# Optimization experiments

Measured on AMD Instinct MI355X. Metric: run time of the kernel, lower is better.

The kernel has to match this reference:

```python
import jax, jax.numpy as jnp
import numpy as np

N, E = 50000, 800000
D, H = 256, 256
OA, OS, OE = 21, 2, 5


def _sage(x, src, dst, wl, bl, wr):
    # PyG SAGEConv: out = lin_l(mean_{j in N(i)} x_j) + lin_r(x_i); bias lives in lin_l
    n = x.shape[0]
    msg = x[src]                                            # [E, d] gather
    agg = jax.ops.segment_sum(msg, dst, num_segments=n)     # [N, d]
    cnt = jax.ops.segment_sum(jnp.ones((src.shape[0],), x.dtype), dst, num_segments=n)
    mean = agg / jnp.maximum(cnt, 1.0)[:, None]
    return mean @ wl.T + bl + x @ wr.T


def _bn(x, g, b, eps=1e-5):
    mu = x.mean(axis=0)
    var = x.var(axis=0)
    return (x - mu) * jax.lax.rsqrt(var + eps) * g + b


def setup_inputs() -> dict:
    key = jax.random.key(0)
    ks = jax.random.split(key, 32)

    def lin(k, o, i):
        s = 1.0 / np.sqrt(i)
        k1, k2 = jax.random.split(k)
        return (jax.random.uniform(k1, (o, i), jnp.float32, -s, s),
                jax.random.uniform(k2, (o,), jnp.float32, -s, s))

    w1l, b1 = lin(ks[3], H, D); w1r, _ = lin(ks[4], H, D)
    w2l, b2 = lin(ks[5], H, H); w2r, _ = lin(ks[6], H, H)
    w3l, b3 = lin(ks[7], H, H); w3r, _ = lin(ks[8], H, H)
    wal, ba = lin(ks[9], OA, H); war, _ = lin(ks[10], OA, H)
    wsl, bs = lin(ks[11], OS, H); wsr, _ = lin(ks[12], OS, H)
    wel, be = lin(ks[13], OE, H); wer, _ = lin(ks[14], OE, H)

    return {
        'x': jax.random.normal(ks[0], (N, D), jnp.float32),
        'edge_src': jax.random.randint(ks[1], (E,), 0, N),
        'edge_dst': jax.random.randint(ks[2], (E,), 0, N),
        'w1l': w1l, 'b1': b1, 'w1r': w1r, 'g1': jnp.ones((H,), jnp.float32), 'bt1': jnp.zeros((H,), jnp.float32),
        'w2l': w2l, 'b2': b2, 'w2r': w2r, 'g2': jnp.ones((H,), jnp.float32), 'bt2': jnp.zeros((H,), jnp.float32),
        'w3l': w3l, 'b3': b3, 'w3r': w3r, 'g3': jnp.ones((H,), jnp.float32), 'bt3': jnp.zeros((H,), jnp.float32),
        'wal': wal, 'ba': ba, 'war': war,
        'wsl': wsl, 'bs': bs, 'wsr': wsr,
        'wel': wel, 'be': be, 'wer': wer,
    }


def reference(x, edge_src, edge_dst,
              w1l, b1, w1r, g1, bt1,
              w2l, b2, w2r, g2, bt2,
              w3l, b3, w3r, g3, bt3,
              wal, ba, war, wsl, bs, wsr, wel, be, wer):
    h = jax.nn.relu(_bn(_sage(x, edge_src, edge_dst, w1l, b1, w1r), g1, bt1))
    h = jax.nn.relu(_bn(_sage(h, edge_src, edge_dst, w2l, b2, w2r), g2, bt2))
    h = jax.nn.relu(_bn(_sage(h, edge_src, edge_dst, w3l, b3, w3r), g3, bt3))
    # dropout is identity in eval mode
    age = _sage(h, edge_src, edge_dst, wal, ba, war)
    sex = _sage(h, edge_src, edge_dst, wsl, bs, wsr)
    eth = _sage(h, edge_src, edge_dst, wel, be, wer)
    return age, sex, eth
```

## Files before the change

kernel.cpp:

```cpp
#include <hip/hip_runtime.h>
#include <hip/hip_bf16.h>
#include <cstddef>

#define HD 256
#define KD 512
#define NH 28

typedef __attribute__((ext_vector_type(8))) short bf16x8;
typedef __attribute__((ext_vector_type(4))) float f32x4;

__device__ inline float bf2f(unsigned short u) { return __uint_as_float(((unsigned)u) << 16); }
__device__ inline unsigned short f2bf(float f) {
    __hip_bfloat16 h = __float2bfloat16(f);
    return *(unsigned short*)&h;
}
__device__ inline float qmax_col(float g, float bt) { return fmaxf(bt + 5.2f * fabsf(g), 1e-6f); }
#define XLO  (-5.5f)
#define XRNG (11.0f)

__global__ void hist_kernel(const int* __restrict__ dst, int* __restrict__ cnt, int E) {
    int e = blockIdx.x * blockDim.x + threadIdx.x;
    if (e < E) atomicAdd(&cnt[dst[e]], 1);
}

__global__ void chunk_reduce_kernel(const int* __restrict__ cnt, int* __restrict__ bsum, int n) {
    __shared__ int sdata[4];
    int idx = blockIdx.x * 256 + threadIdx.x;
    int v = (idx < n) ? ((cnt[idx] + 7) & ~7) : 0;
    for (int off = 32; off > 0; off >>= 1) v += __shfl_down(v, off, 64);
    int lane = threadIdx.x & 63, wv = threadIdx.x >> 6;
    if (lane == 0) sdata[wv] = v;
    __syncthreads();
    if (threadIdx.x == 0) bsum[blockIdx.x] = sdata[0] + sdata[1] + sdata[2] + sdata[3];
}

__global__ void scan_chunks_kernel(const int* __restrict__ bsum, int* __restrict__ boff,
                                   int nchunks, int* __restrict__ row_ptr_end) {
    int t = threadIdx.x;
    int v = (t < nchunks) ? bsum[t] : 0;
    int lane = t & 63, wv = t >> 6;
    int incl = v;
    for (int off = 1; off < 64; off <<= 1) { int u = __shfl_up(incl, off, 64); if (lane >= off) incl += u; }
    __shared__ int wsum[4];
    if (lane == 63) wsum[wv] = incl;
    __syncthreads();
    int base = 0;
    for (int w2 = 0; w2 < 4; ++w2) if (w2 < wv) base += wsum[w2];
    if (t < nchunks) boff[t] = base + incl - v;
    if (t == nchunks - 1) *row_ptr_end = base + incl;
}

__global__ void scan_final_kernel(const int* __restrict__ cnt, const int* __restrict__ boff,
                                  int* __restrict__ row_ptr, float* __restrict__ invdeg, int n) {
    int idx = blockIdx.x * 256 + threadIdx.x;
    int v = (idx < n) ? cnt[idx] : 0;
    int pv = (v + 7) & ~7;
    int lane = threadIdx.x & 63, wv = threadIdx.x >> 6;
    int incl = pv;
    for (int off = 1; off < 64; off <<= 1) { int u = __shfl_up(incl, off, 64); if (lane >= off) incl += u; }
    __shared__ int wsum[4];
    if (lane == 63) wsum[wv] = incl;
    __syncthreads();
    int base = 0;
    for (int w2 = 0; w2 < 4; ++w2) if (w2 < wv) base += wsum[w2];
    if (idx < n) {
        row_ptr[idx] = boff[blockIdx.x] + base + incl - pv;
        invdeg[idx] = 1.0f / fmaxf((float)v, 1.0f);
    }
}

__global__ void scatter_kernel(const int* __restrict__ src, const int* __restrict__ dst,
                               const int* __restrict__ row_ptr, int* __restrict__ cursor,
                               int* __restrict__ col_idx, int E) {
    int e = blockIdx.x * blockDim.x + threadIdx.x;
    if (e < E) {
        int d = dst[e];
        int pos = atomicAdd(&cursor[d], 1);
        col_idx[row_ptr[d] + pos] = src[e];
    }
}

__global__ void fill_pad_kernel(const int* __restrict__ cnt, const int* __restrict__ row_ptr,
                                int* __restrict__ col_idx, int n) {
    int idx = blockIdx.x * 256 + threadIdx.x;
    if (idx >= n) return;
    int s = row_ptr[idx] + cnt[idx];
    int e = row_ptr[idx + 1];
    for (; s < e; ++s) col_idx[s] = n;
}

__global__ void pack_all(const float* __restrict__ w1l, const float* __restrict__ w1r,
                         const float* __restrict__ w2l, const float* __restrict__ w2r,
                         const float* __restrict__ w3l, const float* __restrict__ w3r,
                         const float* __restrict__ wal, const float* __restrict__ war,
                         const float* __restrict__ wsl, const float* __restrict__ wsr,
                         const float* __restrict__ wel, const float* __restrict__ wer,
                         const float* __restrict__ ba, const float* __restrict__ bs,
                         const float* __restrict__ be,
                         unsigned short* __restrict__ wc1, unsigned short* __restrict__ wc2,
                         unsigned short* __restrict__ wc3, unsigned short* __restrict__ w2h,
                         float* __restrict__ bcat) {
    int idx = blockIdx.x * 256 + threadIdx.x;
    if (idx < 3 * HD * KD) {
        int l = idx / (HD * KD), r = idx % (HD * KD);
        int nn = r >> 9, k = r & 511;
        const float* L = (l == 0) ? w1l : (l == 1) ? w2l : w3l;
        const float* R = (l == 0) ? w1r : (l == 1) ? w2r : w3r;
        float v = (k < HD) ? L[nn * HD + k] : R[nn * HD + (k - HD)];
        unsigned short* D = (l == 0) ? wc1 : (l == 1) ? wc2 : wc3;
        D[r] = f2bf(v);
        return;
    }
    int r = idx - 3 * HD * KD;
    if (r >= 64 * HD) return;
    int o = r >> 8, k = r & 255;
    float v = 0.f;
    if (o < 21)                    v = wal[o * HD + k];
    else if (o < 23)               v = wsl[(o - 21) * HD + k];
    else if (o < 28)               v = wel[(o - 23) * HD + k];
    else if (o >= 32 && o < 53)    v = war[(o - 32) * HD + k];
    else if (o >= 53 && o < 55)    v = wsr[(o - 53) * HD + k];
    else if (o >= 55 && o < 60)    v = wer[(o - 55) * HD + k];
    w2h[r] = f2bf(v);
    if (k == 0 && o < 32) {
        float b = 0.f;
        if (o < 21) b = ba[o]; else if (o < 23) b = bs[o - 21]; else if (o < 28) b = be[o - 23];
        bcat[o] = b;
    }
}

__global__ void convert_x_kernel(const float* __restrict__ x, unsigned short* __restrict__ buf,
                                 unsigned* __restrict__ q8, int n) {
    int idx = blockIdx.x * 256 + threadIdx.x;
    if (idx >= n * 64) return;
    int r = idx >> 6, c = idx & 63;
    float4 v = ((const float4*)x)[idx];
    ushort4 o;
    o.x = f2bf(v.x); o.y = f2bf(v.y); o.z = f2bf(v.z); o.w = f2bf(v.w);
    *(ushort4*)&buf[(size_t)r * KD + HD + c * 4] = o;
    const float si = 255.f / XRNG;
    unsigned q0 = (unsigned)fminf(fmaxf((v.x - XLO) * si + 0.5f, 0.f), 255.f);
    unsigned q1 = (unsigned)fminf(fmaxf((v.y - XLO) * si + 0.5f, 0.f), 255.f);
    unsigned q2 = (unsigned)fminf(fmaxf((v.z - XLO) * si + 0.5f, 0.f), 255.f);
    unsigned q3 = (unsigned)fminf(fmaxf((v.w - XLO) * si + 0.5f, 0.f), 255.f);
    q8[(size_t)r * 64 + c] = q0 | (q1 << 8) | (q2 << 16) | (q3 << 24);
}

__device__ inline void agg_u8_core(const unsigned* __restrict__ src,
                                   const int* __restrict__ col_idx, int s, int e,
                                   float& fa0, float& fa1, float& fa2, float& fa3) {
    fa0 = fa1 = fa2 = fa3 = 0.f;
    int i = s;
    while (i < e) {
        int ce = i + 256; if (ce > e) ce = e;
        unsigned acc02 = 0, acc13 = 0;
        for (; i < ce; i += 8) {
            int4 ja = *(const int4*)&col_idx[i];
            int4 jb = *(const int4*)&col_idx[i + 4];
            unsigned w0 = src[(size_t)ja.x << 6];
            unsigned w1 = src[(size_t)ja.y << 6];
            unsigned w2 = src[(size_t)ja.z << 6];
            unsigned w3 = src[(size_t)ja.w << 6];
            unsigned w4 = src[(size_t)jb.x << 6];
            unsigned w5 = src[(size_t)jb.y << 6];
            unsigned w6 = src[(size_t)jb.z << 6];
            unsigned w7 = src[(size_t)jb.w << 6];
            acc02 += w0 & 0x00ff00ffu; acc13 += (w0 >> 8) & 0x00ff00ffu;
            acc02 += w1 & 0x00ff00ffu; acc13 += (w1 >> 8) & 0x00ff00ffu;
            acc02 += w2 & 0x00ff00ffu; acc13 += (w2 >> 8) & 0x00ff00ffu;
            acc02 += w3 & 0x00ff00ffu; acc13 += (w3 >> 8) & 0x00ff00ffu;
            acc02 += w4 & 0x00ff00ffu; acc13 += (w4 >> 8) & 0x00ff00ffu;
            acc02 += w5 & 0x00ff00ffu; acc13 += (w5 >> 8) & 0x00ff00ffu;
            acc02 += w6 & 0x00ff00ffu; acc13 += (w6 >> 8) & 0x00ff00ffu;
            acc02 += w7 & 0x00ff00ffu; acc13 += (w7 >> 8) & 0x00ff00ffu;
        }
        fa0 += (float)(acc02 & 0xffffu); fa2 += (float)(acc02 >> 16);
        fa1 += (float)(acc13 & 0xffffu); fa3 += (float)(acc13 >> 16);
    }
}

__global__ __launch_bounds__(256) void agg_mean_u8x(unsigned short* __restrict__ buf,
                                                    const unsigned* __restrict__ q8,
                                                    const int* __restrict__ row_ptr,
                                                    const int* __restrict__ col_idx,
                                                    const float* __restrict__ invdeg, int n) {
    int wv = threadIdx.x >> 6, lane = threadIdx.x & 63;
    int node = blockIdx.x * 4 + wv;
    if (node >= n) return;
    int s = row_ptr[node], e = row_ptr[node + 1];
    float fa0, fa1, fa2, fa3;
    agg_u8_core(q8 + lane, col_idx, s, e, fa0, fa1, fa2, fa3);
    float inv = invdeg[node] * (XRNG / 255.f);
    float off = (s < e) ? XLO : 0.f;
    ushort4 o;
    o.x = f2bf(fa0 * inv + off);
    o.y = f2bf(fa1 * inv + off);
    o.z = f2bf(fa2 * inv + off);
    o.w = f2bf(fa3 * inv + off);
    *(ushort4*)&buf[(size_t)node * KD + lane * 4] = o;
}

__global__ __launch_bounds__(256) void agg_mean_u8h(unsigned short* __restrict__ buf,
                                                    const unsigned* __restrict__ q8,
                                                    const int* __restrict__ row_ptr,
                                                    const int* __restrict__ col_idx,
                                                    const float* __restrict__ invdeg,
                                                    const float* __restrict__ g,
                                                    const float* __restrict__ bt, int n) {
    int wv = threadIdx.x >> 6, lane = threadIdx.x & 63;
    int node = blockIdx.x * 4 + wv;
    if (node >= n) return;
    int s = row_ptr[node], e = row_ptr[node + 1];
    float fa0, fa1, fa2, fa3;
    agg_u8_core(q8 + lane, col_idx, s, e, fa0, fa1, fa2, fa3);
    int c4 = lane * 4;
    float4 gg = *(const float4*)&g[c4];
    float4 bb = *(const float4*)&bt[c4];
    float inv = invdeg[node] * (1.f / 255.f);
    ushort4 o;
    o.x = f2bf(fa0 * (qmax_col(gg.x, bb.x) * inv));
    o.y = f2bf(fa1 * (qmax_col(gg.y, bb.y) * inv));
    o.z = f2bf(fa2 * (qmax_col(gg.z, bb.z) * inv));
    o.w = f2bf(fa3 * (qmax_col(gg.w, bb.w) * inv));
    *(ushort4*)&buf[(size_t)node * KD + c4] = o;
}

#define SWIZ(row, kc) (((row) << 6) + ((((kc) ^ ((row) & 7))) << 3))

__global__ __launch_bounds__(256) void gemm_mfma_stats(
        const unsigned short* __restrict__ A, const unsigned short* __restrict__ W,
        unsigned short* __restrict__ Zb,
        float* __restrict__ colsum, float* __restrict__ colsumsq, int n) {
    __shared__ __align__(16) short As[128 * 64];
    __shared__ __align__(16) short Bs[128 * 64];
    int t = threadIdx.x;
    int wave = t >> 6, lane = t & 63;
    int wm = wave & 1, wn = wave >> 1;
    int lm = lane & 15, q = lane >> 4;
    int r0 = blockIdx.x * 128, c0 = blockIdx.y * 128;

    f32x4 acc[4][4];
#pragma unroll
    for (int i = 0; i < 4; ++i)
#pragma unroll
        for (int j = 0; j < 4; ++j) acc[i][j] = (f32x4){0.f, 0.f, 0.f, 0.f};

    int srow = t >> 3;
    int skc = t & 7;

    for (int kt = 0; kt < 8; ++kt) {
        int kc = kt * 64;
#pragma unroll
        for (int u = 0; u < 4; ++u) {
            int row = srow + u * 32;
            int ga = r0 + row; if (ga >= n) ga = n - 1;
            *(float4*)&As[SWIZ(row, skc)] = *(const float4*)&A[(size_t)ga * KD + kc + skc * 8];
            *(float4*)&Bs[SWIZ(row, skc)] = *(const float4*)&W[(size_t)(c0 + row) * KD + kc + skc * 8];
        }
        __syncthreads();
#pragma unroll
        for (int kk = 0; kk < 2; ++kk) {
            bf16x8 af[4], bfv[4];
#pragma unroll
            for (int i = 0; i < 4; ++i)
                af[i] = *(bf16x8*)&As[SWIZ(wm * 64 + i * 16 + lm, kk * 4 + q)];
#pragma unroll
            for (int j = 0; j < 4; ++j)
                bfv[j] = *(bf16x8*)&Bs[SWIZ(wn * 64 + j * 16 + lm, kk * 4 + q)];
#pragma unroll
            for (int i = 0; i < 4; ++i)
#pragma unroll
                for (int j = 0; j < 4; ++j)
                    acc[i][j] = __builtin_amdgcn_mfma_f32_16x16x32_bf16(af[i], bfv[j], acc[i][j], 0, 0, 0);
        }
        __syncthreads();
    }

    float s[4], s2[4];
#pragma unroll
    for (int j = 0; j < 4; ++j) { s[j] = 0.f; s2[j] = 0.f; }
#pragma unroll
    for (int i = 0; i < 4; ++i) {
        int rbase = r0 + wm * 64 + i * 16 + q * 4;
#pragma unroll
        for (int reg = 0; reg < 4; ++reg) {
            int r = rbase + reg;
            if (r < n) {
#pragma unroll
                for (int j = 0; j < 4; ++j) {
                    float v = acc[i][j][reg];
                    int c = c0 + wn * 64 + j * 16 + lm;
                    Zb[(size_t)r * KD + HD + c] = f2bf(v);
                    s[j] += v; s2[j] += v * v;
                }
            }
        }
    }
#pragma unroll
    for (int j = 0; j < 4; ++j) {
        s[j]  += __shfl_xor(s[j], 16, 64);  s[j]  += __shfl_xor(s[j], 32, 64);
        s2[j] += __shfl_xor(s2[j], 16, 64); s2[j] += __shfl_xor(s2[j], 32, 64);
    }
    float* red = (float*)As;
    if (t < 128) { red[t * 2] = 0.f; red[t * 2 + 1] = 0.f; }
    __syncthreads();
    if (lane < 16) {
#pragma unroll
        for (int j = 0; j < 4; ++j) {
            int cl = wn * 64 + j * 16 + lm;
            atomicAdd(&red[cl * 2], s[j]);
            atomicAdd(&red[cl * 2 + 1], s2[j]);
        }
    }
    __syncthreads();
    if (t < 128) {
        atomicAdd(&colsum[c0 + t], red[t * 2]);
        atomicAdd(&colsumsq[c0 + t], red[t * 2 + 1]);
    }
}

__global__ void bn_apply_relu_kernel(unsigned short* __restrict__ buf, unsigned* __restrict__ q8,
                                     const float* __restrict__ colsum, const float* __restrict__ colsumsq,
                                     const float* __restrict__ g, const float* __restrict__ bt,
                                     int total4, int n, int w8) {
    int idx = blockIdx.x * blockDim.x + threadIdx.x;
    if (idx >= total4) return;
    int r = idx >> 6, c = idx & 63;
    int c4 = c * 4;
    float fn = (float)n;
    float4 cs = *(const float4*)&colsum[c4];
    float4 cq = *(const float4*)&colsumsq[c4];
    float4 gg = *(const float4*)&g[c4];
    float4 bb = *(const float4*)&bt[c4];
    float mu, var, sc0, sc1, sc2, sc3, sh0, sh1, sh2, sh3;
    mu = cs.x / fn; var = cq.x / fn - mu * mu; sc0 = gg.x * rsqrtf(var + 1e-5f); sh0 = bb.x - mu * sc0;
    mu = cs.y / fn; var = cq.y / fn - mu * mu; sc1 = gg.y * rsqrtf(var + 1e-5f); sh1 = bb.y - mu * sc1;
    mu = cs.z / fn; var = cq.z / fn - mu * mu; sc2 = gg.z * rsqrtf(var + 1e-5f); sh2 = bb.z - mu * sc2;
    mu = cs.w / fn; var = cq.w / fn - mu * mu; sc3 = gg.w * rsqrtf(var + 1e-5f); sh3 = bb.w - mu * sc3;
    unsigned short* p = &buf[(size_t)r * KD + HD + c4];
    ushort4 z = *(ushort4*)p;
    float h0 = fmaxf(bf2f(z.x) * sc0 + sh0, 0.f);
    float h1 = fmaxf(bf2f(z.y) * sc1 + sh1, 0.f);
    float h2 = fmaxf(bf2f(z.z) * sc2 + sh2, 0.f);
    float h3 = fmaxf(bf2f(z.w) * sc3 + sh3, 0.f);
    ushort4 o;
    o.x = f2bf(h0); o.y = f2bf(h1); o.z = f2bf(h2); o.w = f2bf(h3);
    *(ushort4*)p = o;
    if (w8) {
        float si0 = 255.f / qmax_col(gg.x, bb.x);
        float si1 = 255.f / qmax_col(gg.y, bb.y);
        float si2 = 255.f / qmax_col(gg.z, bb.z);
        float si3 = 255.f / qmax_col(gg.w, bb.w);
        unsigned q0 = (unsigned)fminf(h0 * si0 + 0.5f, 255.f);
        unsigned q1 = (unsigned)fminf(h1 * si1 + 0.5f, 255.f);
        unsigned q2 = (unsigned)fminf(h2 * si2 + 0.5f, 255.f);
        unsigned q3 = (unsigned)fminf(h3 * si3 + 0.5f, 255.f);
        q8[(size_t)r * 64 + c] = q0 | (q1 << 8) | (q2 << 16) | (q3 << 24);
    }
}

__global__ __launch_bounds__(256) void heads_pgemm(const unsigned short* __restrict__ A,
                                                   const unsigned short* __restrict__ W2,
                                                   unsigned short* __restrict__ PL,
                                                   unsigned short* __restrict__ PR, int n) {
    __shared__ __align__(16) short As[128 * 64];
    __shared__ __align__(16) short Bs[64 * 64];
    int t = threadIdx.x;
    int wave = t >> 6, lane = t & 63;
    int lm = lane & 15, q = lane >> 4;
    int r0 = blockIdx.x * 128;

    f32x4 acc[2][4];
#pragma unroll
    for (int i = 0; i < 2; ++i)
#pragma unroll
        for (int j = 0; j < 4; ++j) acc[i][j] = (f32x4){0.f, 0.f, 0.f, 0.f};

    int srow = t >> 3;
    int skc = t & 7;

    for (int kt = 0; kt < 4; ++kt) {
        int kc = kt * 64;
#pragma unroll
        for (int u = 0; u < 4; ++u) {
            int row = srow + u * 32;
            int ga = r0 + row; if (ga >= n) ga = n - 1;
            *(float4*)&As[SWIZ(row, skc)] = *(const float4*)&A[(size_t)ga * KD + kc + skc * 8];
        }
#pragma unroll
        for (int u = 0; u < 2; ++u) {
            int c = t + u * 256;
            int row = c >> 3, kcc = c & 7;
            *(float4*)&Bs[SWIZ(row, kcc)] = *(const float4*)&W2[(size_t)row * HD + kc + kcc * 8];
        }
        __syncthreads();
#pragma unroll
        for (int kk = 0; kk < 2; ++kk) {
            bf16x8 af[2], bfv[4];
#pragma unroll
            for (int i = 0; i < 2; ++i)
                af[i] = *(bf16x8*)&As[SWIZ(wave * 32 + i * 16 + lm, kk * 4 + q)];
#pragma unroll
            for (int j = 0; j < 4; ++j)
                bfv[j] = *(bf16x8*)&Bs[SWIZ(j * 16 + lm, kk * 4 + q)];
#pragma unroll
            for (int i = 0; i < 2; ++i)
#pragma unroll
                for (int j = 0; j < 4; ++j)
                    acc[i][j] = __builtin_amdgcn_mfma_f32_16x16x32_bf16(af[i], bfv[j], acc[i][j], 0, 0, 0);
        }
        __syncthreads();
    }
#pragma unroll
    for (int i = 0; i < 2; ++i) {
        int rbase = r0 + wave * 32 + i * 16 + q * 4;
#pragma unroll
        for (int reg = 0; reg < 4; ++reg) {
            int r = rbase + reg;
            if (r >= n) continue;
#pragma unroll
            for (int j = 0; j < 4; ++j) {
                int c = j * 16 + lm;
                unsigned short v = f2bf(acc[i][j][reg]);
                if (c < 32) PL[(size_t)r * 32 + c] = v;
                else        PR[(size_t)r * 32 + (c - 32)] = v;
            }
        }
    }
}

__global__ void head_agg(const unsigned short* __restrict__ PL, const unsigned short* __restrict__ PR,
                         const int* __restrict__ row_ptr, const int* __restrict__ col_idx,
                         const float* __restrict__ invdeg, const float* __restrict__ bcat,
                         float* __restrict__ out, int n) {
    int t = threadIdx.x;
    int sub = t >> 4;
    int l16 = t & 15;
    int node = blockIdx.x * 16 + sub;
    if (node >= n) return;
    int s = row_ptr[node], e = row_ptr[node + 1];
    int off = l16 * 2;
    float a0 = 0.f, a1 = 0.f;
    for (int i = s; i < e; i += 4) {
        int s0 = col_idx[i], s1 = col_idx[i + 1], s2 = col_idx[i + 2], s3 = col_idx[i + 3];
        unsigned v0 = *(const unsigned*)&PL[(size_t)s0 * 32 + off];
        unsigned v1 = *(const unsigned*)&PL[(size_t)s1 * 32 + off];
        unsigned v2 = *(const unsigned*)&PL[(size_t)s2 * 32 + off];
        unsigned v3 = *(const unsigned*)&PL[(size_t)s3 * 32 + off];
        a0 += bf2f((unsigned short)v0) + bf2f((unsigned short)v1) + bf2f((unsigned short)v2) + bf2f((unsigned short)v3);
        a1 += bf2f((unsigned short)(v0 >> 16)) + bf2f((unsigned short)(v1 >> 16))
            + bf2f((unsigned short)(v2 >> 16)) + bf2f((unsigned short)(v3 >> 16));
    }
    float inv = invdeg[node];
    unsigned vr = *(const unsigned*)&PR[(size_t)node * 32 + off];
    float o0 = a0 * inv + bf2f((unsigned short)vr) + bcat[off];
    float o1 = a1 * inv + bf2f((unsigned short)(vr >> 16)) + bcat[off + 1];
    int c0 = off, c1 = off + 1;
    if (c0 < 21)      out[(size_t)node * 21 + c0] = o0;
    else if (c0 < 23) out[(size_t)n * 21 + (size_t)node * 2 + (c0 - 21)] = o0;
    else if (c0 < 28) out[(size_t)n * 23 + (size_t)node * 5 + (c0 - 23)] = o0;
    if (c1 < 21)      out[(size_t)node * 21 + c1] = o1;
    else if (c1 < 23) out[(size_t)n * 21 + (size_t)node * 2 + (c1 - 21)] = o1;
    else if (c1 < 28) out[(size_t)n * 23 + (size_t)node * 5 + (c1 - 23)] = o1;
}

static inline char* align256(char* p) {
    return (char*)(((uintptr_t)p + 255) & ~(uintptr_t)255);
}

extern "C" void kernel_launch(void* const* d_in, const int* in_sizes, int n_in,
                              void* d_out, int out_size, void* d_ws, size_t ws_size,
                              hipStream_t stream) {
    const float* x    = (const float*)d_in[0];
    const int*   esrc = (const int*)d_in[1];
    const int*   edst = (const int*)d_in[2];
    const float* w1l = (const float*)d_in[3];  const float* w1r = (const float*)d_in[5];
    const float* g1  = (const float*)d_in[6];  const float* bt1 = (const float*)d_in[7];
    const float* w2l = (const float*)d_in[8];  const float* w2r = (const float*)d_in[10];
    const float* g2  = (const float*)d_in[11]; const float* bt2 = (const float*)d_in[12];
    const float* w3l = (const float*)d_in[13]; const float* w3r = (const float*)d_in[15];
    const float* g3  = (const float*)d_in[16]; const float* bt3 = (const float*)d_in[17];
    const float* wal = (const float*)d_in[18]; const float* ba = (const float*)d_in[19];
    const float* war = (const float*)d_in[20];
    const float* wsl = (const float*)d_in[21]; const float* bs = (const float*)d_in[22];
    const float* wsr = (const float*)d_in[23];
    const float* wel = (const float*)d_in[24]; const float* be = (const float*)d_in[25];
    const float* wer = (const float*)d_in[26];
    float* out = (float*)d_out;

    int N = in_sizes[0] / HD;
    int E = in_sizes[1];

    char* p = (char*)d_ws;
    size_t HB = (size_t)(N + 1) * KD * sizeof(unsigned short);
    unsigned short* buf0 = (unsigned short*)p; p += HB;
    unsigned short* buf1 = (unsigned short*)p; p += HB;
    p = align256(p);
    unsigned* q8 = (unsigned*)p; p += (size_t)(N + 1) * 64 * sizeof(unsigned);
    p = align256(p);
    unsigned short* PLb = (unsigned short*)p; p += (size_t)(N + 1) * 32 * sizeof(unsigned short);
    unsigned short* PRb = (unsigned short*)p; p += (size_t)N * 32 * sizeof(unsigned short);
    p = align256(p);
    int* col_idx = (int*)p; p += sizeof(int) * ((size_t)E + 8 * (size_t)N + 64);  p = align256(p);
    int* row_ptr = (int*)p; p += sizeof(int) * (size_t)(N + 1); p = align256(p);
    int* cnt     = (int*)p; p += sizeof(int) * (size_t)N;
    int* cursor  = (int*)p; p += sizeof(int) * (size_t)N;       p = align256(p);
    int* bsum    = (int*)p; p += sizeof(int) * 256;
    int* boff    = (int*)p; p += sizeof(int) * 256;             p = align256(p);
    float* invdeg = (float*)p; p += sizeof(float) * (size_t)N;  p = align256(p);
    float* stats  = (float*)p; p += sizeof(float) * 3 * 512;
    p = align256(p);
    unsigned short* wc1 = (unsigned short*)p; p += sizeof(unsigned short) * HD * KD;
    unsigned short* wc2 = (unsigned short*)p; p += sizeof(unsigned short) * HD * KD;
    unsigned short* wc3 = (unsigned short*)p; p += sizeof(unsigned short) * HD * KD;
    unsigned short* w2h = (unsigned short*)p; p += sizeof(unsigned short) * 64 * HD;
    p = align256(p);
    float* bcat = (float*)p; p += sizeof(float) * 32;
    (void)ws_size; (void)n_in; (void)out_size;

    float* zs[3]; float* zq[3];
    for (int l = 0; l < 3; ++l) { zs[l] = stats + l * 512; zq[l] = stats + l * 512 + 256; }

    int nchunks = (N + 255) / 256;

    hipMemsetAsync(cnt, 0, sizeof(int) * 2 * (size_t)N, stream);
    hipMemsetAsync(q8 + (size_t)N * 64, 0, 256, stream);
    hipMemsetAsync(PLb + (size_t)N * 32, 0, 64, stream);
    hipMemsetAsync(stats, 0, sizeof(float) * 3 * 512, stream);
    hist_kernel<<<(E + 255) / 256, 256, 0, stream>>>(edst, cnt, E);
    chunk_reduce_kernel<<<nchunks, 256, 0, stream>>>(cnt, bsum, N);
    scan_chunks_kernel<<<1, 256, 0, stream>>>(bsum, boff, nchunks, &row_ptr[N]);
    scan_final_kernel<<<nchunks, 256, 0, stream>>>(cnt, boff, row_ptr, invdeg, N);
    scatter_kernel<<<(E + 255) / 256, 256, 0, stream>>>(esrc, edst, row_ptr, cursor, col_idx, E);
    fill_pad_kernel<<<nchunks, 256, 0, stream>>>(cnt, row_ptr, col_idx, N);
    pack_all<<<(3 * HD * KD + 64 * HD + 255) / 256, 256, 0, stream>>>(
        w1l, w1r, w2l, w2r, w3l, w3r, wal, war, wsl, wsr, wel, wer,
        ba, bs, be, wc1, wc2, wc3, w2h, bcat);
    convert_x_kernel<<<(N * 64 + 255) / 256, 256, 0, stream>>>(x, buf0, q8, N);

    int aggGrid = (N + 3) / 4;
    dim3 gemmGrid((N + 127) / 128, 2);
    int total4 = N * 64;

    unsigned short* cur = buf0;
    unsigned short* nxt = buf1;
    const unsigned short* wcs[3] = {wc1, wc2, wc3};
    const float* gs[3]  = {g1, g2, g3};
    const float* bts[3] = {bt1, bt2, bt3};

    for (int l = 0; l < 3; ++l) {
        if (l == 0)
            agg_mean_u8x<<<aggGrid, 256, 0, stream>>>(cur, q8, row_ptr, col_idx, invdeg, N);
        else
            agg_mean_u8h<<<aggGrid, 256, 0, stream>>>(cur, q8, row_ptr, col_idx, invdeg,
                                                      gs[l - 1], bts[l - 1], N);
        gemm_mfma_stats<<<gemmGrid, 256, 0, stream>>>(cur, wcs[l], nxt, zs[l], zq[l], N);
        bn_apply_relu_kernel<<<(total4 + 255) / 256, 256, 0, stream>>>(nxt, q8, zs[l], zq[l],
                                                                       gs[l], bts[l], total4, N,
                                                                       (l < 2) ? 1 : 0);
        unsigned short* t2 = cur; cur = nxt; nxt = t2;
    }

    heads_pgemm<<<(N + 127) / 128, 256, 0, stream>>>(cur + HD, w2h, PLb, PRb, N);
    head_agg<<<(N + 15) / 16, 256, 0, stream>>>(PLb, PRb, row_ptr, col_idx, invdeg, bcat, out, N);
}
```

Baseline: 524.7 us.

## Store CSR column indices as 16-bit and register-prefetch GEMM tiles

Column indices are narrowed from int32 to uint16, which halves index traffic in the aggregation and head kernels and allows a single 16-byte load of eight indices. This only works because N=50000 fits in 16 bits, so the code would break for graphs with more than 65535 nodes. The GEMM main loop also gains register double-buffering: the next K-slice of A and W is loaded into registers while the current slice is computed from shared memory. That prefetch costs extra registers and may lower occupancy.

```diff
diff --git a/kernel.cpp b/kernel.cpp
--- a/kernel.cpp
+++ b/kernel.cpp
@@ -7,6 +7,7 @@
 #define NH 28
 
 typedef __attribute__((ext_vector_type(8))) short bf16x8;
+typedef __attribute__((ext_vector_type(8))) unsigned short u16x8;
 typedef __attribute__((ext_vector_type(4))) float f32x4;
 
 __device__ inline float bf2f(unsigned short u) { return __uint_as_float(((unsigned)u) << 16); }
@@ -71,22 +72,23 @@
 
 __global__ void scatter_kernel(const int* __restrict__ src, const int* __restrict__ dst,
                                const int* __restrict__ row_ptr, int* __restrict__ cursor,
-                               int* __restrict__ col_idx, int E) {
+                               unsigned short* __restrict__ col_idx, int E) {
     int e = blockIdx.x * blockDim.x + threadIdx.x;
     if (e < E) {
         int d = dst[e];
         int pos = atomicAdd(&cursor[d], 1);
-        col_idx[row_ptr[d] + pos] = src[e];
+        col_idx[row_ptr[d] + pos] = (unsigned short)src[e];
     }
 }
 
 __global__ void fill_pad_kernel(const int* __restrict__ cnt, const int* __restrict__ row_ptr,
-                                int* __restrict__ col_idx, int n) {
+                                unsigned short* __restrict__ col_idx, int n) {
     int idx = blockIdx.x * 256 + threadIdx.x;
     if (idx >= n) return;
     int s = row_ptr[idx] + cnt[idx];
     int e = row_ptr[idx + 1];
-    for (; s < e; ++s) col_idx[s] = n;
+    unsigned short dn = (unsigned short)n;
+    for (; s < e; ++s) col_idx[s] = dn;
 }
 
 __global__ void pack_all(const float* __restrict__ w1l, const float* __restrict__ w1r,
@@ -147,7 +149,7 @@
 }
 
 __device__ inline void agg_u8_core(const unsigned* __restrict__ src,
-                                   const int* __restrict__ col_idx, int s, int e,
+                                   const unsigned short* __restrict__ col_idx, int s, int e,
                                    float& fa0, float& fa1, float& fa2, float& fa3) {
     fa0 = fa1 = fa2 = fa3 = 0.f;
     int i = s;
@@ -155,16 +157,15 @@
         int ce = i + 256; if (ce > e) ce = e;
         unsigned acc02 = 0, acc13 = 0;
         for (; i < ce; i += 8) {
-            int4 ja = *(const int4*)&col_idx[i];
-            int4 jb = *(const int4*)&col_idx[i + 4];
-            unsigned w0 = src[(size_t)ja.x << 6];
-            unsigned w1 = src[(size_t)ja.y << 6];
-            unsigned w2 = src[(size_t)ja.z << 6];
-            unsigned w3 = src[(size_t)ja.w << 6];
-            unsigned w4 = src[(size_t)jb.x << 6];
-            unsigned w5 = src[(size_t)jb.y << 6];
-            unsigned w6 = src[(size_t)jb.z << 6];
-            unsigned w7 = src[(size_t)jb.w << 6];
+            u16x8 j = *(const u16x8*)&col_idx[i];
+            unsigned w0 = src[(size_t)j[0] << 6];
+            unsigned w1 = src[(size_t)j[1] << 6];
+            unsigned w2 = src[(size_t)j[2] << 6];
+            unsigned w3 = src[(size_t)j[3] << 6];
+            unsigned w4 = src[(size_t)j[4] << 6];
+            unsigned w5 = src[(size_t)j[5] << 6];
+            unsigned w6 = src[(size_t)j[6] << 6];
+            unsigned w7 = src[(size_t)j[7] << 6];
             acc02 += w0 & 0x00ff00ffu; acc13 += (w0 >> 8) & 0x00ff00ffu;
             acc02 += w1 & 0x00ff00ffu; acc13 += (w1 >> 8) & 0x00ff00ffu;
             acc02 += w2 & 0x00ff00ffu; acc13 += (w2 >> 8) & 0x00ff00ffu;
@@ -182,7 +183,7 @@
 __global__ __launch_bounds__(256) void agg_mean_u8x(unsigned short* __restrict__ buf,
                                                     const unsigned* __restrict__ q8,
                                                     const int* __restrict__ row_ptr,
-                                                    const int* __restrict__ col_idx,
+                                                    const unsigned short* __restrict__ col_idx,
                                                     const float* __restrict__ invdeg, int n) {
     int wv = threadIdx.x >> 6, lane = threadIdx.x & 63;
     int node = blockIdx.x * 4 + wv;
@@ -203,7 +204,7 @@
 __global__ __launch_bounds__(256) void agg_mean_u8h(unsigned short* __restrict__ buf,
                                                     const unsigned* __restrict__ q8,
                                                     const int* __restrict__ row_ptr,
-                                                    const int* __restrict__ col_idx,
+                                                    const unsigned short* __restrict__ col_idx,
                                                     const float* __restrict__ invdeg,
                                                     const float* __restrict__ g,
                                                     const float* __restrict__ bt, int n) {
@@ -247,17 +248,38 @@
 
     int srow = t >> 3;
     int skc = t & 7;
+    const unsigned short* aptr[4];
+    const unsigned short* bptr[4];
+#pragma unroll
+    for (int u = 0; u < 4; ++u) {
+        int row = srow + u * 32;
+        int ga = r0 + row; if (ga >= n) ga = n - 1;
+        aptr[u] = &A[(size_t)ga * KD + skc * 8];
+        bptr[u] = &W[(size_t)(c0 + row) * KD + skc * 8];
+    }
+    float4 ra[4], rb[4];
+#pragma unroll
+    for (int u = 0; u < 4; ++u) {
+        ra[u] = *(const float4*)aptr[u];
+        rb[u] = *(const float4*)bptr[u];
+    }
 
     for (int kt = 0; kt < 8; ++kt) {
-        int kc = kt * 64;
 #pragma unroll
         for (int u = 0; u < 4; ++u) {
             int row = srow + u * 32;
-            int ga = r0 + row; if (ga >= n) ga = n - 1;
-            *(float4*)&As[SWIZ(row, skc)] = *(const float4*)&A[(size_t)ga * KD + kc + skc * 8];
-            *(float4*)&Bs[SWIZ(row, skc)] = *(const float4*)&W[(size_t)(c0 + row) * KD + kc + skc * 8];
+            *(float4*)&As[SWIZ(row, skc)] = ra[u];
+            *(float4*)&Bs[SWIZ(row, skc)] = rb[u];
         }
         __syncthreads();
+        if (kt < 7) {
+            int kc = (kt + 1) * 64;
+#pragma unroll
+            for (int u = 0; u < 4; ++u) {
+                ra[u] = *(const float4*)(aptr[u] + kc);
+                rb[u] = *(const float4*)(bptr[u] + kc);
+            }
+        }
 #pragma unroll
         for (int kk = 0; kk < 2; ++kk) {
             bf16x8 af[4], bfv[4];
@@ -430,7 +452,7 @@
 }
 
 __global__ void head_agg(const unsigned short* __restrict__ PL, const unsigned short* __restrict__ PR,
-                         const int* __restrict__ row_ptr, const int* __restrict__ col_idx,
+                         const int* __restrict__ row_ptr, const unsigned short* __restrict__ col_idx,
                          const float* __restrict__ invdeg, const float* __restrict__ bcat,
                          float* __restrict__ out, int n) {
     int t = threadIdx.x;
@@ -442,11 +464,11 @@
     int off = l16 * 2;
     float a0 = 0.f, a1 = 0.f;
     for (int i = s; i < e; i += 4) {
-        int s0 = col_idx[i], s1 = col_idx[i + 1], s2 = col_idx[i + 2], s3 = col_idx[i + 3];
-        unsigned v0 = *(const unsigned*)&PL[(size_t)s0 * 32 + off];
-        unsigned v1 = *(const unsigned*)&PL[(size_t)s1 * 32 + off];
-        unsigned v2 = *(const unsigned*)&PL[(size_t)s2 * 32 + off];
-        unsigned v3 = *(const unsigned*)&PL[(size_t)s3 * 32 + off];
+        ushort4 jj = *(const ushort4*)&col_idx[i];
+        unsigned v0 = *(const unsigned*)&PL[(size_t)jj.x * 32 + off];
+        unsigned v1 = *(const unsigned*)&PL[(size_t)jj.y * 32 + off];
+        unsigned v2 = *(const unsigned*)&PL[(size_t)jj.z * 32 + off];
+        unsigned v3 = *(const unsigned*)&PL[(size_t)jj.w * 32 + off];
         a0 += bf2f((unsigned short)v0) + bf2f((unsigned short)v1) + bf2f((unsigned short)v2) + bf2f((unsigned short)v3);
         a1 += bf2f((unsigned short)(v0 >> 16)) + bf2f((unsigned short)(v1 >> 16))
             + bf2f((unsigned short)(v2 >> 16)) + bf2f((unsigned short)(v3 >> 16));
@@ -501,7 +523,8 @@
     unsigned short* PLb = (unsigned short*)p; p += (size_t)(N + 1) * 32 * sizeof(unsigned short);
     unsigned short* PRb = (unsigned short*)p; p += (size_t)N * 32 * sizeof(unsigned short);
     p = align256(p);
-    int* col_idx = (int*)p; p += sizeof(int) * ((size_t)E + 8 * (size_t)N + 64);  p = align256(p);
+    unsigned short* col_idx = (unsigned short*)p;
+    p += sizeof(unsigned short) * ((size_t)E + 8 * (size_t)N + 64);             p = align256(p);
     int* row_ptr = (int*)p; p += sizeof(int) * (size_t)(N + 1); p = align256(p);
     int* cnt     = (int*)p; p += sizeof(int) * (size_t)N;
     int* cursor  = (int*)p; p += sizeof(int) * (size_t)N;       p = align256(p);
```

After: 661.1 us. +26.0%, slower.
